# Kernel optimization log

Measured on AMD Instinct MI355X. Metric: run time of the kernel, lower is better.

## Reference

```python
import jax, jax.numpy as jnp
import numpy as np

EMPHASIS_FACTOR = 1.5
TOP_K_PERCENT = 0.2


def setup_inputs() -> dict:
    key = jax.random.key(0)
    k1, k2 = jax.random.split(key)
    B, S, D = 32, 8192, 256
    x = jax.random.normal(k1, (B, S, D), dtype=jnp.float32)
    W = jax.random.normal(k2, (D, 1), dtype=jnp.float32) * (1.0 / np.sqrt(D))
    b = jnp.zeros((1,), dtype=jnp.float32)
    return {"x": x, "W": W, "b": b}


def reference(x, W, b):
    B, S, D = x.shape
    # e = tanh(x @ W + b): [B, S, 1]
    e = jnp.tanh(jnp.einsum('bsd,do->bso', x, W) + b)
    # softmax over seq axis, squeeze -> [B, S]
    a = jax.nn.softmax(e, axis=1)[..., 0]
    # top-k selection: k = max(1, int(S * top_k_percent)), static under jit
    k = max(1, int(S * TOP_K_PERCENT))
    _, top_k_idx = jax.lax.top_k(a, k)  # [B, k]
    # mask of top-k positions (equiv to one_hot + reduce_max, but a direct scatter)
    mask = jnp.zeros((B, S), dtype=bool).at[jnp.arange(B)[:, None], top_k_idx].set(True)
    emphasized_a = jnp.where(mask, a * EMPHASIS_FACTOR, a)  # [B, S]
    # weighted sum over seq -> [B, D]
    summed_output = jnp.einsum('bsd,bs->bd', x, emphasized_a)
    return summed_output, emphasized_a
```

## Files before the change

### kernel.cpp

```cpp
#include <hip/hip_runtime.h>
#include <math.h>

#define BB 32
#define SS 8192
#define DD 256
#define K_SEL 1638
#define EMPH 1.5f
#define HBINS 2048
#define HCH 8
#define IDX_STRIDE 1664
#define K5_BLOCKS 8
#define K5_SLICE 205
#define NCHUNK 64
#define ROWS_PER_BLOCK (SS / NCHUNK)

__device__ __forceinline__ unsigned monokey(float f) {
    unsigned u = __float_as_uint(f);
    return u ^ ((u & 0x80000000u) ? 0xFFFFFFFFu : 0x80000000u);
}

__global__ __launch_bounds__(1024) void k1_e_hist_s1(const float* __restrict__ x,
                                                     const float* __restrict__ W,
                                                     const float* __restrict__ bias,
                                                     float* __restrict__ e_ws,
                                                     unsigned* __restrict__ hist_ws,
                                                     float* __restrict__ s1part) {
    __shared__ unsigned hist[HBINS];
    __shared__ float red[16 * 256];
    const int tid = threadIdx.x;
    const int lane = tid & 63;
    const int wv = tid >> 6;
    for (int i = tid; i < HBINS; i += 1024) hist[i] = 0;

    const int b = blockIdx.x >> 3;
    const int ch = blockIdx.x & 7;
    const int row0 = ch * 1024;

    const float4* W4 = (const float4*)W;
    const int cg = lane & 15;
    const float4 w0 = W4[cg];
    const float4 w1 = W4[cg + 16];
    const float4 w2 = W4[cg + 32];
    const float4 w3 = W4[cg + 48];
    const float bias0 = bias[0];
    __syncthreads();

    const float* xb = x + (size_t)b * SS * DD;
    float* eb = e_ws + (size_t)b * SS;

    float acc[16];
    #pragma unroll
    for (int m = 0; m < 16; m++) acc[m] = 0.0f;

    for (int it = 0; it < 16; it++) {
        const int r = row0 + (it * 16 + wv) * 4 + (lane >> 4);
        const float4* rp = (const float4*)(xb + (size_t)r * DD);
        float4 a0 = rp[cg];
        float4 a1 = rp[cg + 16];
        float4 a2 = rp[cg + 32];
        float4 a3 = rp[cg + 48];
        float p = a0.x * w0.x + a0.y * w0.y + a0.z * w0.z + a0.w * w0.w;
        p += a1.x * w1.x + a1.y * w1.y + a1.z * w1.z + a1.w * w1.w;
        p += a2.x * w2.x + a2.y * w2.y + a2.z * w2.z + a2.w * w2.w;
        p += a3.x * w3.x + a3.y * w3.y + a3.z * w3.z + a3.w * w3.w;
        p += __shfl_xor(p, 1, 64);
        p += __shfl_xor(p, 2, 64);
        p += __shfl_xor(p, 4, 64);
        p += __shfl_xor(p, 8, 64);
        float ev = tanhf(p + bias0);
        float w = expf(ev);
        if (cg == 0) {
            eb[r] = ev;
            atomicAdd(&hist[monokey(ev) >> 21], 1u);
        }
        acc[0] += w * a0.x;  acc[1] += w * a0.y;  acc[2] += w * a0.z;  acc[3] += w * a0.w;
        acc[4] += w * a1.x;  acc[5] += w * a1.y;  acc[6] += w * a1.z;  acc[7] += w * a1.w;
        acc[8] += w * a2.x;  acc[9] += w * a2.y;  acc[10] += w * a2.z; acc[11] += w * a2.w;
        acc[12] += w * a3.x; acc[13] += w * a3.y; acc[14] += w * a3.z; acc[15] += w * a3.w;
    }
    #pragma unroll
    for (int m = 0; m < 16; m++) {
        acc[m] += __shfl_xor(acc[m], 16, 64);
        acc[m] += __shfl_xor(acc[m], 32, 64);
    }
    if (lane < 16) {
        #pragma unroll
        for (int m = 0; m < 16; m++) red[wv * 256 + lane * 16 + m] = acc[m];
    }
    __syncthreads();
    unsigned* hout = hist_ws + (size_t)blockIdx.x * HBINS;
    for (int i = tid; i < HBINS; i += 1024) hout[i] = hist[i];
    if (tid < 256) {
        const int d = tid;
        const int q = d >> 6;
        const int cg2 = (d >> 2) & 15;
        const int j = d & 3;
        const int m = q * 4 + j;
        float s = 0.0f;
        #pragma unroll
        for (int w = 0; w < 16; w++) s += red[w * 256 + cg2 * 16 + m];
        s1part[(size_t)blockIdx.x * DD + d] = s;
    }
}

__global__ __launch_bounds__(1024) void k2_select(const float* __restrict__ e_ws,
                                                  const unsigned* __restrict__ hist_ws,
                                                  float* __restrict__ ea_out,
                                                  float* __restrict__ zinv,
                                                  int* __restrict__ idx_ws) {
    const int b = blockIdx.x;
    const int tid = threadIdx.x;
    const int lane = tid & 63;
    const int wid = tid >> 6;

    __shared__ float se[SS];
    __shared__ float wredf[16];
    __shared__ unsigned binTot[HBINS];
    __shared__ unsigned gsuf[256];
    __shared__ unsigned h7[128];
    __shared__ unsigned wcnt[16];
    __shared__ unsigned uvar[3];
    __shared__ unsigned selCnt;
    __shared__ float fvar[1];

    const float* eg = e_ws + (size_t)b * SS;
    float* og = ea_out + (size_t)b * SS;
    int* il = idx_ws + (size_t)b * IDX_STRIDE;

    float lsum = 0.0f;
    #pragma unroll
    for (int i = 0; i < 8; i++) {
        int s = tid + i * 1024;
        float v = eg[s];
        se[s] = v;
        lsum += expf(v);
    }
    #pragma unroll
    for (int off = 32; off >= 1; off >>= 1)
        lsum += __shfl_xor(lsum, off, 64);
    if (lane == 0) wredf[wid] = lsum;

    unsigned c0 = 0, c1 = 0;
    for (int ch = 0; ch < HCH; ch++) {
        const unsigned* hc = hist_ws + ((size_t)(b * HCH + ch)) * HBINS;
        c0 += hc[2 * tid];
        c1 += hc[2 * tid + 1];
    }
    binTot[2 * tid] = c0;
    binTot[2 * tid + 1] = c1;
    if (tid == 0) selCnt = 0;
    __syncthreads();

    if (tid == 0) {
        float z = 0.0f;
        for (int w = 0; w < 16; w++) z += wredf[w];
        fvar[0] = 1.0f / z;
        zinv[b] = fvar[0];
    }
    if (tid < 256) {
        unsigned g = 0;
        #pragma unroll
        for (int j = 0; j < 8; j++) g += binTot[tid * 8 + j];
        gsuf[tid] = g;
    }
    __syncthreads();
    for (int off = 1; off < 256; off <<= 1) {
        unsigned add = 0;
        if (tid < 256 && tid + off < 256) add = gsuf[tid + off];
        __syncthreads();
        if (tid < 256) gsuf[tid] += add;
        __syncthreads();
    }
    if (tid < 256) {
        unsigned above = (tid == 255) ? 0u : gsuf[tid + 1];
        if (above < K_SEL && K_SEL <= gsuf[tid]) {
            unsigned running = above;
            for (int j = 7; j >= 0; j--) {
                int bin = tid * 8 + j;
                unsigned c = binTot[bin];
                if (running < K_SEL && K_SEL <= running + c) {
                    uvar[0] = (unsigned)bin;
                    uvar[1] = K_SEL - running;
                    break;
                }
                running += c;
            }
        }
    }
    __syncthreads();
    unsigned prefix = uvar[0];
    unsigned kk = uvar[1];

    #pragma unroll
    for (int pass = 0; pass < 3; pass++) {
        const int shift = 14 - 7 * pass;
        if (tid < 128) h7[tid] = 0;
        __syncthreads();
        #pragma unroll
        for (int i = 0; i < 8; i++) {
            unsigned key = monokey(se[tid + i * 1024]);
            if ((key >> (shift + 7)) == prefix)
                atomicAdd(&h7[(key >> shift) & 127u], 1u);
        }
        __syncthreads();
        for (int off = 1; off < 128; off <<= 1) {
            unsigned add = 0;
            if (tid < 128 && tid + off < 128) add = h7[tid + off];
            __syncthreads();
            if (tid < 128) h7[tid] += add;
            __syncthreads();
        }
        if (tid < 128) {
            unsigned above = (tid == 127) ? 0u : h7[tid + 1];
            if (above < kk && kk <= h7[tid]) {
                uvar[0] = (prefix << 7) | (unsigned)tid;
                uvar[1] = kk - above;
            }
        }
        __syncthreads();
        prefix = uvar[0];
        kk = uvar[1];
        __syncthreads();
    }
    const unsigned T = prefix;
    const unsigned r = kk;
    const float invZ = fvar[0];

    if (tid == 0) uvar[2] = 0;
    __syncthreads();
    for (int chunk = 0; chunk < 8; chunk++) {
        int s = chunk * 1024 + tid;
        float v = se[s];
        unsigned key = monokey(v);
        bool gt = key > T;
        bool eq = (key == T);
        unsigned long long bal = __ballot(eq);
        unsigned waveTot = (unsigned)__popcll(bal);
        unsigned myPref = (unsigned)__popcll(bal & ((1ull << lane) - 1ull));
        if (lane == 0) wcnt[wid] = waveTot;
        __syncthreads();
        unsigned base = uvar[2];
        for (int w = 0; w < wid; w++) base += wcnt[w];
        bool sel = gt || (eq && (base + myPref) < r);
        float a = expf(v) * invZ;
        og[s] = sel ? a * EMPH : a;
        if (sel) {
            unsigned slot = atomicAdd(&selCnt, 1u);
            il[slot] = s;
        }
        __syncthreads();
        if (tid == 0) {
            unsigned t = uvar[2];
            for (int w = 0; w < 16; w++) t += wcnt[w];
            uvar[2] = t;
        }
        __syncthreads();
    }
}

__global__ __launch_bounds__(256) void k5_corr(const float* __restrict__ x,
                                               const float* __restrict__ ea,
                                               const int* __restrict__ idx_ws,
                                               float* __restrict__ corr) {
    const int b = blockIdx.x >> 3;
    const int j = blockIdx.x & 7;
    const int lane = threadIdx.x & 63;
    const int wid = threadIdx.x >> 6;
    const int lo = j * K5_SLICE;
    const int hi = (lo + K5_SLICE < K_SEL) ? lo + K5_SLICE : K_SEL;
    const int* il = idx_ws + (size_t)b * IDX_STRIDE;
    const float* xb = x + (size_t)b * SS * DD;
    const float* ab = ea + (size_t)b * SS;
    float4 acc = make_float4(0.f, 0.f, 0.f, 0.f);
    for (int t = lo + wid; t < hi; t += 4) {
        int s = il[t];
        float w = ab[s] * (1.0f / 3.0f);
        float4 x4 = ((const float4*)(xb + (size_t)s * DD))[lane];
        acc.x += w * x4.x; acc.y += w * x4.y; acc.z += w * x4.z; acc.w += w * x4.w;
    }
    __shared__ float lds[4 * 256];
    ((float4*)lds)[wid * 64 + lane] = acc;
    __syncthreads();
    const int t = threadIdx.x;
    float v = lds[t] + lds[256 + t] + lds[512 + t] + lds[768 + t];
    corr[(size_t)blockIdx.x * DD + t] = v;
}

__global__ __launch_bounds__(256) void k6_final(const float* __restrict__ s1part,
                                                const float* __restrict__ corr,
                                                const float* __restrict__ zinv,
                                                float* __restrict__ out) {
    const int b = blockIdx.x;
    const int d = threadIdx.x;
    float s1 = 0.0f;
    #pragma unroll
    for (int ch = 0; ch < HCH; ch++) s1 += s1part[((size_t)b * HCH + ch) * DD + d];
    float c = 0.0f;
    #pragma unroll
    for (int j = 0; j < K5_BLOCKS; j++) c += corr[((size_t)b * K5_BLOCKS + j) * DD + d];
    out[b * DD + d] = s1 * zinv[b] + c;
}

__global__ __launch_bounds__(256) void f1_dot_tanh(const float* __restrict__ x,
                                                   const float* __restrict__ W,
                                                   const float* __restrict__ bias,
                                                   float* __restrict__ e) {
    const int lane = threadIdx.x & 63;
    const int wib  = threadIdx.x >> 6;
    const int waveId = blockIdx.x * 4 + wib;
    const int totalWaves = gridDim.x * 4;
    const float4 w4 = ((const float4*)W)[lane];
    const float bias0 = bias[0];
    for (int row = waveId; row < BB * SS; row += totalWaves) {
        float4 x4 = ((const float4*)(x + (size_t)row * DD))[lane];
        float p = x4.x * w4.x + x4.y * w4.y + x4.z * w4.z + x4.w * w4.w;
        #pragma unroll
        for (int off = 32; off >= 1; off >>= 1)
            p += __shfl_xor(p, off, 64);
        if (lane == 0) e[row] = tanhf(p + bias0);
    }
}
__global__ __launch_bounds__(1024) void f2_softmax_topk(float* __restrict__ ea) {
    const int b = blockIdx.x;
    const int tid = threadIdx.x;
    const int lane = tid & 63;
    const int wid  = tid >> 6;
    __shared__ float se[SS];
    __shared__ float wredf[16];
    __shared__ unsigned hist[256];
    __shared__ unsigned ssum[256];
    __shared__ unsigned wcnt[16];
    __shared__ unsigned uvar[3];
    __shared__ float fvar[1];
    float* eg = ea + (size_t)b * SS;
    float lsum = 0.0f;
    #pragma unroll
    for (int i = 0; i < 8; i++) {
        int s = tid + i * 1024;
        float v = eg[s];
        se[s] = v;
        lsum += expf(v);
    }
    #pragma unroll
    for (int off = 32; off >= 1; off >>= 1)
        lsum += __shfl_xor(lsum, off, 64);
    if (lane == 0) wredf[wid] = lsum;
    __syncthreads();
    if (tid == 0) {
        float z = 0.0f;
        for (int w = 0; w < 16; w++) z += wredf[w];
        fvar[0] = 1.0f / z;
    }
    __syncthreads();
    const float invZ = fvar[0];
    unsigned kk = K_SEL;
    unsigned prefix = 0;
    for (int byte = 3; byte >= 0; byte--) {
        if (tid < 256) hist[tid] = 0;
        __syncthreads();
        #pragma unroll
        for (int i = 0; i < 8; i++) {
            unsigned key = monokey(se[tid + i * 1024]);
            bool active = (byte == 3) || ((key >> ((byte + 1) * 8)) == prefix);
            if (active) atomicAdd(&hist[(key >> (byte * 8)) & 0xFFu], 1u);
        }
        __syncthreads();
        if (tid < 256) ssum[tid] = hist[tid];
        __syncthreads();
        for (int off = 1; off < 256; off <<= 1) {
            unsigned add = 0;
            if (tid < 256 && tid + off < 256) add = ssum[tid + off];
            __syncthreads();
            if (tid < 256) ssum[tid] += add;
            __syncthreads();
        }
        if (tid < 256) {
            unsigned above = (tid == 255) ? 0u : ssum[tid + 1];
            if (above < kk && kk <= ssum[tid]) {
                uvar[0] = (unsigned)tid;
                uvar[1] = kk - above;
            }
        }
        __syncthreads();
        prefix = (prefix << 8) | uvar[0];
        kk = uvar[1];
        __syncthreads();
    }
    const unsigned T = prefix;
    const unsigned r = kk;
    if (tid == 0) uvar[2] = 0;
    __syncthreads();
    for (int chunk = 0; chunk < 8; chunk++) {
        int s = chunk * 1024 + tid;
        float v = se[s];
        unsigned key = monokey(v);
        bool gt = key > T;
        bool eq = (key == T);
        unsigned long long bal = __ballot(eq);
        unsigned waveTot = (unsigned)__popcll(bal);
        unsigned myPref = (unsigned)__popcll(bal & ((1ull << lane) - 1ull));
        if (lane == 0) wcnt[wid] = waveTot;
        __syncthreads();
        unsigned base = uvar[2];
        for (int w = 0; w < wid; w++) base += wcnt[w];
        bool sel = gt || (eq && (base + myPref) < r);
        float a = expf(v) * invZ;
        eg[s] = sel ? a * EMPH : a;
        __syncthreads();
        if (tid == 0) {
            unsigned t = uvar[2];
            for (int w = 0; w < 16; w++) t += wcnt[w];
            uvar[2] = t;
        }
        __syncthreads();
    }
}
__global__ __launch_bounds__(256) void f0_zero(float* __restrict__ p, int n) {
    int i = blockIdx.x * blockDim.x + threadIdx.x;
    if (i < n) p[i] = 0.0f;
}
__global__ __launch_bounds__(256) void f3_weighted_atomic(const float* __restrict__ x,
                                                          const float* __restrict__ ea,
                                                          float* __restrict__ out) {
    const int blk = blockIdx.x;
    const int b = blk / NCHUNK;
    const int chunk = blk % NCHUNK;
    const int lane = threadIdx.x & 63;
    const int wid  = threadIdx.x >> 6;
    const float* xb = x + ((size_t)b * SS + (size_t)chunk * ROWS_PER_BLOCK) * DD;
    const float* ab = ea + (size_t)b * SS + (size_t)chunk * ROWS_PER_BLOCK;
    float4 acc = make_float4(0.f, 0.f, 0.f, 0.f);
    for (int rr = wid; rr < ROWS_PER_BLOCK; rr += 4) {
        float4 x4 = ((const float4*)(xb + (size_t)rr * DD))[lane];
        float a = ab[rr];
        acc.x += x4.x * a; acc.y += x4.y * a; acc.z += x4.z * a; acc.w += x4.w * a;
    }
    __shared__ float lds[4 * 256];
    ((float4*)lds)[wid * 64 + lane] = acc;
    __syncthreads();
    const int t = threadIdx.x;
    float v = lds[t] + lds[256 + t] + lds[512 + t] + lds[768 + t];
    atomicAdd(&out[b * 256 + t], v);
}

extern "C" void kernel_launch(void* const* d_in, const int* in_sizes, int n_in,
                              void* d_out, int out_size, void* d_ws, size_t ws_size,
                              hipStream_t stream) {
    (void)in_sizes; (void)n_in; (void)out_size;
    const float* x    = (const float*)d_in[0];
    const float* W    = (const float*)d_in[1];
    const float* bias = (const float*)d_in[2];
    float* out = (float*)d_out;
    float* sum_out = out;
    float* ea = out + BB * DD;

    const size_t e_bytes    = (size_t)BB * SS * sizeof(float);
    const size_t hist_bytes = (size_t)BB * HCH * HBINS * sizeof(unsigned);
    const size_t s1_bytes   = (size_t)BB * HCH * DD * sizeof(float);
    const size_t corr_bytes = (size_t)BB * K5_BLOCKS * DD * sizeof(float);
    const size_t zinv_bytes = 128;
    const size_t idx_bytes  = (size_t)BB * IDX_STRIDE * sizeof(int);
    const size_t need = e_bytes + hist_bytes + s1_bytes + corr_bytes + zinv_bytes + idx_bytes;

    if (ws_size >= need) {
        char* p = (char*)d_ws;
        float*    e_ws    = (float*)p;                 p += e_bytes;
        unsigned* hist_ws = (unsigned*)p;              p += hist_bytes;
        float*    s1part  = (float*)p;                 p += s1_bytes;
        float*    corr    = (float*)p;                 p += corr_bytes;
        float*    zinv    = (float*)p;                 p += zinv_bytes;
        int*      idx_ws  = (int*)p;

        k1_e_hist_s1<<<BB * HCH, 1024, 0, stream>>>(x, W, bias, e_ws, hist_ws, s1part);
        k2_select<<<BB, 1024, 0, stream>>>(e_ws, hist_ws, ea, zinv, idx_ws);
        k5_corr<<<BB * K5_BLOCKS, 256, 0, stream>>>(x, ea, idx_ws, corr);
        k6_final<<<BB, 256, 0, stream>>>(s1part, corr, zinv, sum_out);
    } else {
        f1_dot_tanh<<<4096, 256, 0, stream>>>(x, W, bias, ea);
        f2_softmax_topk<<<BB, 1024, 0, stream>>>(ea);
        f0_zero<<<(BB * DD + 255) / 256, 256, 0, stream>>>(sum_out, BB * DD);
        f3_weighted_atomic<<<BB * NCHUNK, 256, 0, stream>>>(x, ea, sum_out);
    }
}
```

Measured before the change: 403.6 us.

## Move softmax denominator into k1 and replace barrier-heavy scans with wave scans

k1 now accumulates the per-chunk sum of exp(e) and writes it to a small partial buffer, so k2 no longer recomputes exp over all 8192 elements to get the normaliser. In k2, the shared-memory suffix scans that used a __syncthreads per step are replaced by single-wave shuffle scans. The tie-rank pass over the 8 chunks is restructured to precompute per-wave equal counts with a prefix scan, which removes the per-chunk barriers. The main cost targeted is latency in the single-block-per-batch select kernel. The float sum order changes slightly and k1 gains an LDS atomic.

```diff
diff --git a/kernel.cpp b/kernel.cpp
--- a/kernel.cpp
+++ b/kernel.cpp
@@ -24,13 +24,16 @@
                                                      const float* __restrict__ bias,
                                                      float* __restrict__ e_ws,
                                                      unsigned* __restrict__ hist_ws,
-                                                     float* __restrict__ s1part) {
+                                                     float* __restrict__ s1part,
+                                                     float* __restrict__ zpart) {
     __shared__ unsigned hist[HBINS];
     __shared__ float red[16 * 256];
+    __shared__ float zred;
     const int tid = threadIdx.x;
     const int lane = tid & 63;
     const int wv = tid >> 6;
     for (int i = tid; i < HBINS; i += 1024) hist[i] = 0;
+    if (tid == 0) zred = 0.0f;
 
     const int b = blockIdx.x >> 3;
     const int ch = blockIdx.x & 7;
@@ -51,6 +54,7 @@
     float acc[16];
     #pragma unroll
     for (int m = 0; m < 16; m++) acc[m] = 0.0f;
+    float zloc = 0.0f;
 
     for (int it = 0; it < 16; it++) {
         const int r = row0 + (it * 16 + wv) * 4 + (lane >> 4);
@@ -72,6 +76,7 @@
         if (cg == 0) {
             eb[r] = ev;
             atomicAdd(&hist[monokey(ev) >> 21], 1u);
+            zloc += w;
         }
         acc[0] += w * a0.x;  acc[1] += w * a0.y;  acc[2] += w * a0.z;  acc[3] += w * a0.w;
         acc[4] += w * a1.x;  acc[5] += w * a1.y;  acc[6] += w * a1.z;  acc[7] += w * a1.w;
@@ -83,6 +88,9 @@
         acc[m] += __shfl_xor(acc[m], 16, 64);
         acc[m] += __shfl_xor(acc[m], 32, 64);
     }
+    zloc += __shfl_xor(zloc, 16, 64);
+    zloc += __shfl_xor(zloc, 32, 64);
+    if (lane == 0) atomicAdd(&zred, zloc);
     if (lane < 16) {
         #pragma unroll
         for (int m = 0; m < 16; m++) red[wv * 256 + lane * 16 + m] = acc[m];
@@ -90,6 +98,7 @@
     __syncthreads();
     unsigned* hout = hist_ws + (size_t)blockIdx.x * HBINS;
     for (int i = tid; i < HBINS; i += 1024) hout[i] = hist[i];
+    if (tid == 0) zpart[blockIdx.x] = zred;
     if (tid < 256) {
         const int d = tid;
         const int q = d >> 6;
@@ -105,6 +114,7 @@
 
 __global__ __launch_bounds__(1024) void k2_select(const float* __restrict__ e_ws,
                                                   const unsigned* __restrict__ hist_ws,
+                                                  const float* __restrict__ zpart,
                                                   float* __restrict__ ea_out,
                                                   float* __restrict__ zinv,
                                                   int* __restrict__ idx_ws) {
@@ -114,32 +124,33 @@
     const int wid = tid >> 6;
 
     __shared__ float se[SS];
-    __shared__ float wredf[16];
     __shared__ unsigned binTot[HBINS];
-    __shared__ unsigned gsuf[256];
+    __shared__ unsigned gsuf[257];
+    __shared__ unsigned hsuf[129];
     __shared__ unsigned h7[128];
-    __shared__ unsigned wcnt[16];
-    __shared__ unsigned uvar[3];
+    __shared__ unsigned ecnt[128];
+    __shared__ unsigned ebase[128];
+    __shared__ unsigned uvar[2];
     __shared__ unsigned selCnt;
-    __shared__ float fvar[1];
+    __shared__ float fvar;
 
     const float* eg = e_ws + (size_t)b * SS;
     float* og = ea_out + (size_t)b * SS;
     int* il = idx_ws + (size_t)b * IDX_STRIDE;
 
-    float lsum = 0.0f;
     #pragma unroll
     for (int i = 0; i < 8; i++) {
         int s = tid + i * 1024;
-        float v = eg[s];
-        se[s] = v;
-        lsum += expf(v);
-    }
-    #pragma unroll
-    for (int off = 32; off >= 1; off >>= 1)
-        lsum += __shfl_xor(lsum, off, 64);
-    if (lane == 0) wredf[wid] = lsum;
-
+        se[s] = eg[s];
+    }
+    if (tid == 0) {
+        float z = 0.0f;
+        #pragma unroll
+        for (int c = 0; c < HCH; c++) z += zpart[b * HCH + c];
+        fvar = 1.0f / z;
+        zinv[b] = fvar;
+        selCnt = 0;
+    }
     unsigned c0 = 0, c1 = 0;
     for (int ch = 0; ch < HCH; ch++) {
         const unsigned* hc = hist_ws + ((size_t)(b * HCH + ch)) * HBINS;
@@ -148,38 +159,45 @@
     }
     binTot[2 * tid] = c0;
     binTot[2 * tid + 1] = c1;
-    if (tid == 0) selCnt = 0;
-    __syncthreads();
-
-    if (tid == 0) {
-        float z = 0.0f;
-        for (int w = 0; w < 16; w++) z += wredf[w];
-        fvar[0] = 1.0f / z;
-        zinv[b] = fvar[0];
-    }
+    __syncthreads();
+
+    if (wid == 0) {
+        unsigned g[4];
+        unsigned tot = 0;
+        #pragma unroll
+        for (int j = 0; j < 4; j++) {
+            unsigned s = 0;
+            #pragma unroll
+            for (int m = 0; m < 8; m++) s += binTot[(lane * 4 + j) * 8 + m];
+            g[j] = s;
+            tot += s;
+        }
+        unsigned xx = tot;
+        #pragma unroll
+        for (int off = 1; off < 64; off <<= 1) {
+            unsigned v = __shfl_down(xx, off, 64);
+            if (lane + off < 64) xx += v;
+        }
+        unsigned Snext = __shfl_down(xx, 1, 64);
+        if (lane == 63) Snext = 0;
+        unsigned s3 = Snext + g[3];
+        unsigned s2 = s3 + g[2];
+        unsigned s1 = s2 + g[1];
+        unsigned s0 = s1 + g[0];
+        gsuf[4 * lane] = s0; gsuf[4 * lane + 1] = s1;
+        gsuf[4 * lane + 2] = s2; gsuf[4 * lane + 3] = s3;
+        if (lane == 63) gsuf[256] = 0;
+    }
+    __syncthreads();
+
     if (tid < 256) {
-        unsigned g = 0;
-        #pragma unroll
-        for (int j = 0; j < 8; j++) g += binTot[tid * 8 + j];
-        gsuf[tid] = g;
-    }
-    __syncthreads();
-    for (int off = 1; off < 256; off <<= 1) {
-        unsigned add = 0;
-        if (tid < 256 && tid + off < 256) add = gsuf[tid + off];
-        __syncthreads();
-        if (tid < 256) gsuf[tid] += add;
-        __syncthreads();
-    }
-    if (tid < 256) {
-        unsigned above = (tid == 255) ? 0u : gsuf[tid + 1];
+        unsigned above = gsuf[tid + 1];
         if (above < K_SEL && K_SEL <= gsuf[tid]) {
             unsigned running = above;
             for (int j = 7; j >= 0; j--) {
-                int bin = tid * 8 + j;
-                unsigned c = binTot[bin];
+                unsigned c = binTot[tid * 8 + j];
                 if (running < K_SEL && K_SEL <= running + c) {
-                    uvar[0] = (unsigned)bin;
+                    uvar[0] = (unsigned)(tid * 8 + j);
                     uvar[1] = K_SEL - running;
                     break;
                 }
@@ -203,16 +221,28 @@
                 atomicAdd(&h7[(key >> shift) & 127u], 1u);
         }
         __syncthreads();
-        for (int off = 1; off < 128; off <<= 1) {
-            unsigned add = 0;
-            if (tid < 128 && tid + off < 128) add = h7[tid + off];
-            __syncthreads();
-            if (tid < 128) h7[tid] += add;
-            __syncthreads();
-        }
+        if (wid == 0) {
+            unsigned a0 = h7[2 * lane];
+            unsigned a1 = h7[2 * lane + 1];
+            unsigned tot = a0 + a1;
+            unsigned xx = tot;
+            #pragma unroll
+            for (int off = 1; off < 64; off <<= 1) {
+                unsigned v = __shfl_down(xx, off, 64);
+                if (lane + off < 64) xx += v;
+            }
+            unsigned Snext = __shfl_down(xx, 1, 64);
+            if (lane == 63) Snext = 0;
+            unsigned t1 = Snext + a1;
+            unsigned t0 = t1 + a0;
+            hsuf[2 * lane] = t0;
+            hsuf[2 * lane + 1] = t1;
+            if (lane == 63) hsuf[128] = 0;
+        }
+        __syncthreads();
         if (tid < 128) {
-            unsigned above = (tid == 127) ? 0u : h7[tid + 1];
-            if (above < kk && kk <= h7[tid]) {
+            unsigned above = hsuf[tid + 1];
+            if (above < kk && kk <= hsuf[tid]) {
                 uvar[0] = (prefix << 7) | (unsigned)tid;
                 uvar[1] = kk - above;
             }
@@ -220,41 +250,49 @@
         __syncthreads();
         prefix = uvar[0];
         kk = uvar[1];
-        __syncthreads();
     }
     const unsigned T = prefix;
     const unsigned r = kk;
-    const float invZ = fvar[0];
-
-    if (tid == 0) uvar[2] = 0;
-    __syncthreads();
-    for (int chunk = 0; chunk < 8; chunk++) {
-        int s = chunk * 1024 + tid;
+    const float invZ = fvar;
+
+    #pragma unroll
+    for (int c = 0; c < 8; c++) {
+        int s = c * 1024 + tid;
+        unsigned long long bal = __ballot(monokey(se[s]) == T);
+        if (lane == 0) ecnt[c * 16 + wid] = (unsigned)__popcll(bal);
+    }
+    __syncthreads();
+    if (wid == 0) {
+        unsigned a0 = ecnt[2 * lane];
+        unsigned a1 = ecnt[2 * lane + 1];
+        unsigned tot = a0 + a1;
+        unsigned xx = tot;
+        #pragma unroll
+        for (int off = 1; off < 64; off <<= 1) {
+            unsigned v = __shfl_up(xx, off, 64);
+            if (lane >= off) xx += v;
+        }
+        ebase[2 * lane] = xx - tot;
+        ebase[2 * lane + 1] = xx - a1;
+    }
+    __syncthreads();
+    #pragma unroll
+    for (int c = 0; c < 8; c++) {
+        int s = c * 1024 + tid;
         float v = se[s];
         unsigned key = monokey(v);
-        bool gt = key > T;
         bool eq = (key == T);
+        bool gt = (key > T);
         unsigned long long bal = __ballot(eq);
-        unsigned waveTot = (unsigned)__popcll(bal);
         unsigned myPref = (unsigned)__popcll(bal & ((1ull << lane) - 1ull));
-        if (lane == 0) wcnt[wid] = waveTot;
-        __syncthreads();
-        unsigned base = uvar[2];
-        for (int w = 0; w < wid; w++) base += wcnt[w];
-        bool sel = gt || (eq && (base + myPref) < r);
+        unsigned rank = ebase[c * 16 + wid] + myPref;
+        bool sel = gt || (eq && rank < r);
         float a = expf(v) * invZ;
         og[s] = sel ? a * EMPH : a;
         if (sel) {
             unsigned slot = atomicAdd(&selCnt, 1u);
             il[slot] = s;
         }
-        __syncthreads();
-        if (tid == 0) {
-            unsigned t = uvar[2];
-            for (int w = 0; w < 16; w++) t += wcnt[w];
-            uvar[2] = t;
-        }
-        __syncthreads();
     }
 }
 
@@ -459,8 +497,10 @@
     const size_t s1_bytes   = (size_t)BB * HCH * DD * sizeof(float);
     const size_t corr_bytes = (size_t)BB * K5_BLOCKS * DD * sizeof(float);
     const size_t zinv_bytes = 128;
+    const size_t zpart_bytes= (size_t)BB * HCH * sizeof(float);
     const size_t idx_bytes  = (size_t)BB * IDX_STRIDE * sizeof(int);
-    const size_t need = e_bytes + hist_bytes + s1_bytes + corr_bytes + zinv_bytes + idx_bytes;
+    const size_t need = e_bytes + hist_bytes + s1_bytes + corr_bytes + zinv_bytes
+                      + zpart_bytes + idx_bytes;
 
     if (ws_size >= need) {
         char* p = (char*)d_ws;
@@ -469,10 +509,11 @@
         float*    s1part  = (float*)p;                 p += s1_bytes;
         float*    corr    = (float*)p;                 p += corr_bytes;
         float*    zinv    = (float*)p;                 p += zinv_bytes;
+        float*    zpart   = (float*)p;                 p += zpart_bytes;
         int*      idx_ws  = (int*)p;
 
-        k1_e_hist_s1<<<BB * HCH, 1024, 0, stream>>>(x, W, bias, e_ws, hist_ws, s1part);
-        k2_select<<<BB, 1024, 0, stream>>>(e_ws, hist_ws, ea, zinv, idx_ws);
+        k1_e_hist_s1<<<BB * HCH, 1024, 0, stream>>>(x, W, bias, e_ws, hist_ws, s1part, zpart);
+        k2_select<<<BB, 1024, 0, stream>>>(e_ws, hist_ws, zpart, ea, zinv, idx_ws);
         k5_corr<<<BB * K5_BLOCKS, 256, 0, stream>>>(x, ea, idx_ws, corr);
         k6_final<<<BB, 256, 0, stream>>>(s1part, corr, zinv, sum_out);
     } else {
```

Measured after the change: 398.6 us. No clear change (-1.2%).
